# Kernel tuning notes

Measured on AMD Instinct MI355X. Metric: run time of the kernel, lower is better.

The kernel has to match this reference:

```python
import jax, jax.numpy as jnp
import numpy as np

N, K, D = 131072, 4096, 64


def setup_inputs() -> dict:
    key = jax.random.key(0)
    k1, k2 = jax.random.split(key)
    z_e_x = jax.random.normal(k1, (N, D), dtype=jnp.float32)
    codebook = jax.random.normal(k2, (K, D), dtype=jnp.float32)
    return {"z_e_x": z_e_x, "codebook": codebook}


def reference(z_e_x, codebook):
    inputs_sqr = jnp.sum(z_e_x * z_e_x, axis=1, keepdims=True)       # [N, 1]
    codebook_sqr = jnp.sum(codebook * codebook, axis=1)              # [K]
    distances = inputs_sqr + codebook_sqr - 2.0 * jnp.einsum(
        'nd,kd->nk', z_e_x, codebook)                                # [N, K]
    indices = jnp.argmin(distances, axis=1)                          # [N]
    codes = jnp.take(codebook, indices, axis=0)                      # [N, D]
    # Straight-through path: grads pass to z_e_x, not to codebook
    z_q_x_st = z_e_x + jax.lax.stop_gradient(codes - z_e_x)
    # Differentiable-codebook path (index_select on live weight)
    z_q_x_bar = codes
    return jnp.stack([z_q_x_st, z_q_x_bar])                          # [2, N, D]
```

## Files before the change

### kernel.cpp

```cpp
#include <hip/hip_runtime.h>

typedef __attribute__((ext_vector_type(8))) short short8;
typedef __attribute__((ext_vector_type(4))) float f32x4;

constexpr int N_ROWS = 131072;
constexpr int K_CB   = 4096;
constexpr int D_DIM  = 64;
constexpr float EPS_MARGIN = 2.0e-3f;

constexpr size_t CTR_OFF   = 0;
constexpr size_t CSQ_OFF   = 64;
constexpr size_t CBH_OFF   = 16512;
constexpr size_t CBL_OFF   = CBH_OFF + 524288;
constexpr size_t BESTI_OFF = CBL_OFF + 524288;
constexpr size_t LIST_OFF  = BESTI_OFF + 524288;

#define MFMA(a, b, c) __builtin_amdgcn_mfma_f32_16x16x32_bf16((a), (b), (c), 0, 0, 0)

__device__ __forceinline__ unsigned short f2bf(float f) {
    unsigned int u = __builtin_bit_cast(unsigned int, f);
    u = (u + 0x7fffu + ((u >> 16) & 1u)) >> 16;
    return (unsigned short)u;
}
__device__ __forceinline__ float bf2f(unsigned short h) {
    return __builtin_bit_cast(float, ((unsigned int)h) << 16);
}

__device__ __forceinline__ short8 ldfrag(const unsigned char* smbase, int row, int lane, int ks) {
    const int slot = (((lane >> 4) + ks * 4) ^ (lane & 7));
    uint4 v = *(const uint4*)(smbase + row * 128 + slot * 16);
    return __builtin_bit_cast(short8, v);
}

__global__ __launch_bounds__(256)
void prep_csq(const float* __restrict__ cb, float* __restrict__ csq) {
    const int k = blockIdx.x * 256 + threadIdx.x;
    const float4* row = (const float4*)(cb + (size_t)k * D_DIM);
    float s = 0.f;
    #pragma unroll
    for (int i = 0; i < 16; ++i) {
        float4 v = row[i];
        s = fmaf(v.x, v.x, s); s = fmaf(v.y, v.y, s);
        s = fmaf(v.z, v.z, s); s = fmaf(v.w, v.w, s);
    }
    csq[k] = s;
}

__global__ __launch_bounds__(256)
void prep_split(const float* __restrict__ cb, unsigned char* __restrict__ cbh,
                unsigned char* __restrict__ cbl) {
    const int id  = blockIdx.x * 256 + threadIdx.x;
    const int row = id >> 3, s = id & 7;
    const float4* src = (const float4*)(cb + (size_t)row * D_DIM + s * 8);
    float4 v0 = src[0], v1 = src[1];
    float f[8] = {v0.x, v0.y, v0.z, v0.w, v1.x, v1.y, v1.z, v1.w};
    unsigned int hw[4], lw[4];
    #pragma unroll
    for (int i = 0; i < 4; ++i) {
        unsigned short h0 = f2bf(f[2*i]),     l0 = f2bf(f[2*i]     - bf2f(h0));
        unsigned short h1 = f2bf(f[2*i + 1]), l1 = f2bf(f[2*i + 1] - bf2f(h1));
        hw[i] = (unsigned int)h0 | ((unsigned int)h1 << 16);
        lw[i] = (unsigned int)l0 | ((unsigned int)l1 << 16);
    }
    const int slot = s ^ (row & 7);
    *(uint4*)(cbh + (size_t)row * 128 + slot * 16) = make_uint4(hw[0], hw[1], hw[2], hw[3]);
    *(uint4*)(cbl + (size_t)row * 128 + slot * 16) = make_uint4(lw[0], lw[1], lw[2], lw[3]);
}

__global__ void init_counter(int* counter) { if (threadIdx.x == 0) *counter = 0; }

__device__ __forceinline__ void stage_tile(const unsigned char* __restrict__ cbh,
                                           const unsigned char* __restrict__ cbl,
                                           const float* __restrict__ csqg,
                                           unsigned char* sm, int kt, int wid, int lane) {
    const unsigned char* sh = cbh + (size_t)kt * 128;
    const unsigned char* sl = cbl + (size_t)kt * 128;
    #pragma unroll
    for (int p = 0; p < 4; ++p) {
        const int chunk = wid * 4 + p;
        __builtin_amdgcn_global_load_lds(
            (const __attribute__((address_space(1))) void*)(sh + chunk * 1024 + lane * 16),
            (__attribute__((address_space(3))) void*)(sm + chunk * 1024), 16, 0, 0);
    }
    #pragma unroll
    for (int p = 0; p < 4; ++p) {
        const int chunk = wid * 4 + p;
        __builtin_amdgcn_global_load_lds(
            (const __attribute__((address_space(1))) void*)(sl + chunk * 1024 + lane * 16),
            (__attribute__((address_space(3))) void*)(sm + 16384 + chunk * 1024), 16, 0, 0);
    }
    if (wid < 2) {
        __builtin_amdgcn_global_load_lds(
            (const __attribute__((address_space(1))) void*)(csqg + kt + wid * 64 + lane),
            (__attribute__((address_space(3))) void*)(sm + 32768 + wid * 256), 4, 0, 0);
    }
}

__global__ __launch_bounds__(256, 2)
void vq_main_mfma(const float* __restrict__ z,
                  const float* __restrict__ cb,
                  const unsigned char* __restrict__ cbh,
                  const unsigned char* __restrict__ cbl,
                  const float* __restrict__ csqg,
                  int* __restrict__ besti, int* __restrict__ list,
                  int* __restrict__ counter, float* __restrict__ out) {
    __shared__ __align__(16) unsigned char sm[2][33792];
    const int t = threadIdx.x, lane = t & 63, wid = t >> 6;
    const int n0 = blockIdx.x * 128;
    const int wbase = wid * 32;

    #pragma unroll
    for (int p = 0; p < 4; ++p) {
        const int id = t + p * 256;
        const int row = id >> 3, s = id & 7;
        const float4* src = (const float4*)(z + (size_t)(n0 + row) * D_DIM + s * 8);
        float4 v0 = src[0], v1 = src[1];
        float f[8] = {v0.x, v0.y, v0.z, v0.w, v1.x, v1.y, v1.z, v1.w};
        unsigned int hw[4], lw[4];
        #pragma unroll
        for (int i = 0; i < 4; ++i) {
            unsigned short h0 = f2bf(f[2*i]),     l0 = f2bf(f[2*i]     - bf2f(h0));
            unsigned short h1 = f2bf(f[2*i + 1]), l1 = f2bf(f[2*i + 1] - bf2f(h1));
            hw[i] = (unsigned int)h0 | ((unsigned int)h1 << 16);
            lw[i] = (unsigned int)l0 | ((unsigned int)l1 << 16);
        }
        const int slot = s ^ (row & 7);
        *(uint4*)(&sm[0][row * 128 + slot * 16])         = make_uint4(hw[0], hw[1], hw[2], hw[3]);
        *(uint4*)(&sm[0][16384 + row * 128 + slot * 16]) = make_uint4(lw[0], lw[1], lw[2], lw[3]);
    }
    __syncthreads();

    short8 ah[2][2], al[2][2];
    #pragma unroll
    for (int m = 0; m < 2; ++m)
        #pragma unroll
        for (int ks = 0; ks < 2; ++ks) {
            const int row = wbase + m * 16 + (lane & 15);
            ah[m][ks] = ldfrag(&sm[0][0],     row, lane, ks);
            al[m][ks] = ldfrag(&sm[0][16384], row, lane, ks);
        }
    __syncthreads();

    float b1[2][4], b2[2][4]; int i1[2][4];
    #pragma unroll
    for (int m = 0; m < 2; ++m)
        #pragma unroll
        for (int r = 0; r < 4; ++r) { b1[m][r] = __builtin_inff(); b2[m][r] = __builtin_inff(); i1[m][r] = 0; }

    stage_tile(cbh, cbl, csqg, &sm[0][0], 0, wid, lane);
    __syncthreads();
    int cur = 0;
    for (int kt = 0; kt < K_CB; kt += 128) {
        if (kt + 128 < K_CB)
            stage_tile(cbh, cbl, csqg, &sm[cur ^ 1][0], kt + 128, wid, lane);
        const unsigned char* bhp = &sm[cur][0];
        const unsigned char* blp = &sm[cur][16384];
        const float* cs_l = (const float*)&sm[cur][32768];
        #pragma unroll 2
        for (int c = 0; c < 8; ++c) {
            const int brow = c * 16 + (lane & 15);
            short8 bh0 = ldfrag(bhp, brow, lane, 0), bh1 = ldfrag(bhp, brow, lane, 1);
            short8 bl0 = ldfrag(blp, brow, lane, 0), bl1 = ldfrag(blp, brow, lane, 1);
            const float cs = cs_l[c * 16 + (lane & 15)];
            const int idx = kt + c * 16 + (lane & 15);
            #pragma unroll
            for (int m = 0; m < 2; ++m) {
                f32x4 a0 = {0.f, 0.f, 0.f, 0.f}, a1 = {0.f, 0.f, 0.f, 0.f};
                a0 = MFMA(ah[m][0], bh0, a0);
                a1 = MFMA(ah[m][1], bh1, a1);
                a0 = MFMA(al[m][0], bh0, a0);
                a1 = MFMA(al[m][1], bh1, a1);
                a0 = MFMA(ah[m][0], bl0, a0);
                a1 = MFMA(ah[m][1], bl1, a1);
                a0 = MFMA(al[m][0], bl0, a0);
                a1 = MFMA(al[m][1], bl1, a1);
                #pragma unroll
                for (int r = 0; r < 4; ++r) {
                    const float d = fmaf(a0[r] + a1[r], -2.f, cs);
                    const bool lt = d < b1[m][r];
                    b2[m][r] = fminf(b2[m][r], lt ? b1[m][r] : d);
                    b1[m][r] = lt ? d : b1[m][r];
                    i1[m][r] = lt ? idx : i1[m][r];
                }
            }
        }
        __syncthreads();
        cur ^= 1;
    }

    int* bidx_lds = (int*)&sm[0][0];
    #pragma unroll
    for (int m = 0; m < 2; ++m)
        #pragma unroll
        for (int r = 0; r < 4; ++r) {
            float v1 = b1[m][r], v2 = b2[m][r]; int j1 = i1[m][r];
            #pragma unroll
            for (int msk = 1; msk < 16; msk <<= 1) {
                const float ov1 = __shfl_xor(v1, msk);
                const int   oj1 = __shfl_xor(j1, msk);
                const float ov2 = __shfl_xor(v2, msk);
                const bool take = (ov1 < v1) || (ov1 == v1 && oj1 < j1);
                const float nv2 = fminf(take ? v1 : v2, take ? ov2 : ov1);
                v1 = take ? ov1 : v1; j1 = take ? oj1 : j1; v2 = nv2;
            }
            if ((lane & 15) == 0) {
                const int rloc = wbase + m * 16 + (lane >> 4) * 4 + r;
                const int row = n0 + rloc;
                besti[row] = j1;
                bidx_lds[rloc] = j1;
                if (v2 - v1 < EPS_MARGIN) {
                    const int p = atomicAdd(counter, 1);
                    list[p] = row;
                }
            }
        }
    __syncthreads();

    const float4* cb4 = (const float4*)cb;
    float4* out4 = (float4*)out;
    #pragma unroll
    for (int p = 0; p < 8; ++p) {
        const int id  = t + p * 256;
        const int row = id >> 4, c4 = id & 15;
        const int k = bidx_lds[row];
        const float4 v = cb4[(size_t)k * 16 + c4];
        out4[(size_t)(n0 + row) * 16 + c4] = v;
        out4[(size_t)N_ROWS * 16 + (size_t)(n0 + row) * 16 + c4] = v;
    }
}

__global__ __launch_bounds__(256)
void repair_kernel(const float* __restrict__ z, const float* __restrict__ cb,
                   const float* __restrict__ csq, const int* __restrict__ list,
                   const int* __restrict__ counter, int* __restrict__ besti,
                   float* __restrict__ out) {
    __shared__ float xs[64];
    __shared__ float rv[4];
    __shared__ int   ri[4];
    __shared__ int   fi_s;
    const int cnt = counter[0];
    const int t = threadIdx.x;
    for (int e = blockIdx.x; e < cnt; e += gridDim.x) {
        const int row = list[e];
        __syncthreads();
        if (t < 64) xs[t] = z[(size_t)row * D_DIM + t];
        __syncthreads();
        float bv = __builtin_inff(); int bi = 0x7fffffff;
        for (int k = t; k < K_CB; k += 256) {
            const float4* cr = (const float4*)(cb + (size_t)k * D_DIM);
            float dot = 0.f;
            #pragma unroll
            for (int i = 0; i < 16; ++i) {
                float4 v = cr[i];
                dot = fmaf(v.x, xs[i * 4 + 0], dot);
                dot = fmaf(v.y, xs[i * 4 + 1], dot);
                dot = fmaf(v.z, xs[i * 4 + 2], dot);
                dot = fmaf(v.w, xs[i * 4 + 3], dot);
            }
            const float d = fmaf(dot, -2.f, csq[k]);
            if (d < bv) { bv = d; bi = k; }
        }
        #pragma unroll
        for (int msk = 1; msk < 64; msk <<= 1) {
            const float ov = __shfl_xor(bv, msk);
            const int   oi = __shfl_xor(bi, msk);
            if (ov < bv || (ov == bv && oi < bi)) { bv = ov; bi = oi; }
        }
        if ((t & 63) == 0) { rv[t >> 6] = bv; ri[t >> 6] = bi; }
        __syncthreads();
        if (t == 0) {
            float fb = rv[0]; int fi = ri[0];
            #pragma unroll
            for (int w = 1; w < 4; ++w)
                if (rv[w] < fb || (rv[w] == fb && ri[w] < fi)) { fb = rv[w]; fi = ri[w]; }
            besti[row] = fi;
            fi_s = fi;
        }
        __syncthreads();
        if (t < 32) {
            const int dest = t >> 4, c4 = t & 15;
            const float4 v = ((const float4*)cb)[(size_t)fi_s * 16 + c4];
            float4* dst = (float4*)out + (size_t)dest * N_ROWS * 16 + (size_t)row * 16 + c4;
            *dst = v;
        }
        __syncthreads();
    }
}

extern "C" void kernel_launch(void* const* d_in, const int* in_sizes, int n_in,
                              void* d_out, int out_size, void* d_ws, size_t ws_size,
                              hipStream_t stream) {
    const float* z  = (const float*)d_in[0];
    const float* cb = (const float*)d_in[1];
    float* out = (float*)d_out;
    unsigned char* ws = (unsigned char*)d_ws;

    int*   counter = (int*)(ws + CTR_OFF);
    float* csq     = (float*)(ws + CSQ_OFF);
    unsigned char* cbh = ws + CBH_OFF;
    unsigned char* cbl = ws + CBL_OFF;
    int* besti = (int*)(ws + BESTI_OFF);
    int* list  = (int*)(ws + LIST_OFF);

    prep_csq<<<K_CB / 256, 256, 0, stream>>>(cb, csq);
    prep_split<<<(K_CB * 8) / 256, 256, 0, stream>>>(cb, cbh, cbl);
    init_counter<<<1, 64, 0, stream>>>(counter);
    vq_main_mfma<<<N_ROWS / 128, 256, 0, stream>>>(z, cb, cbh, cbl, csq, besti, list, counter, out);
    repair_kernel<<<1024, 256, 0, stream>>>(z, cb, csq, list, counter, besti, out);
}
```

Before: 287.6 us.

## Drop low*low MFMA term, halve codebook tile and raise occupancy

Result: faster. 255.9 us (-11.0%).

```diff
diff --git a/kernel.cpp b/kernel.cpp
--- a/kernel.cpp
+++ b/kernel.cpp
@@ -6,14 +6,13 @@
 constexpr int N_ROWS = 131072;
 constexpr int K_CB   = 4096;
 constexpr int D_DIM  = 64;
-constexpr float EPS_MARGIN = 2.0e-3f;
+constexpr float EPS_MARGIN = 2.5e-3f;
 
 constexpr size_t CTR_OFF   = 0;
 constexpr size_t CSQ_OFF   = 64;
 constexpr size_t CBH_OFF   = 16512;
 constexpr size_t CBL_OFF   = CBH_OFF + 524288;
-constexpr size_t BESTI_OFF = CBL_OFF + 524288;
-constexpr size_t LIST_OFF  = BESTI_OFF + 524288;
+constexpr size_t LIST_OFF  = CBL_OFF + 524288;
 
 #define MFMA(a, b, c) __builtin_amdgcn_mfma_f32_16x16x32_bf16((a), (b), (c), 0, 0, 0)
 
@@ -76,35 +75,36 @@
     const unsigned char* sh = cbh + (size_t)kt * 128;
     const unsigned char* sl = cbl + (size_t)kt * 128;
     #pragma unroll
-    for (int p = 0; p < 4; ++p) {
-        const int chunk = wid * 4 + p;
+    for (int p = 0; p < 2; ++p) {
+        const int chunk = wid * 2 + p;
         __builtin_amdgcn_global_load_lds(
             (const __attribute__((address_space(1))) void*)(sh + chunk * 1024 + lane * 16),
             (__attribute__((address_space(3))) void*)(sm + chunk * 1024), 16, 0, 0);
     }
     #pragma unroll
-    for (int p = 0; p < 4; ++p) {
-        const int chunk = wid * 4 + p;
+    for (int p = 0; p < 2; ++p) {
+        const int chunk = wid * 2 + p;
         __builtin_amdgcn_global_load_lds(
             (const __attribute__((address_space(1))) void*)(sl + chunk * 1024 + lane * 16),
-            (__attribute__((address_space(3))) void*)(sm + 16384 + chunk * 1024), 16, 0, 0);
-    }
-    if (wid < 2) {
+            (__attribute__((address_space(3))) void*)(sm + 8192 + chunk * 1024), 16, 0, 0);
+    }
+    if (wid == 0) {
         __builtin_amdgcn_global_load_lds(
-            (const __attribute__((address_space(1))) void*)(csqg + kt + wid * 64 + lane),
-            (__attribute__((address_space(3))) void*)(sm + 32768 + wid * 256), 4, 0, 0);
-    }
-}
-
-__global__ __launch_bounds__(256, 2)
+            (const __attribute__((address_space(1))) void*)(csqg + kt + lane),
+            (__attribute__((address_space(3))) void*)(sm + 16384), 4, 0, 0);
+    }
+}
+
+__global__ __launch_bounds__(256, 4)
 void vq_main_mfma(const float* __restrict__ z,
                   const float* __restrict__ cb,
                   const unsigned char* __restrict__ cbh,
                   const unsigned char* __restrict__ cbl,
                   const float* __restrict__ csqg,
-                  int* __restrict__ besti, int* __restrict__ list,
+                  int* __restrict__ list,
                   int* __restrict__ counter, float* __restrict__ out) {
-    __shared__ __align__(16) unsigned char sm[2][33792];
+    __shared__ __align__(16) unsigned char sm[2][16640];
+    unsigned char* smf = &sm[0][0];
     const int t = threadIdx.x, lane = t & 63, wid = t >> 6;
     const int n0 = blockIdx.x * 128;
     const int wbase = wid * 32;
@@ -125,8 +125,8 @@
             lw[i] = (unsigned int)l0 | ((unsigned int)l1 << 16);
         }
         const int slot = s ^ (row & 7);
-        *(uint4*)(&sm[0][row * 128 + slot * 16])         = make_uint4(hw[0], hw[1], hw[2], hw[3]);
-        *(uint4*)(&sm[0][16384 + row * 128 + slot * 16]) = make_uint4(lw[0], lw[1], lw[2], lw[3]);
+        *(uint4*)(smf + row * 128 + slot * 16)         = make_uint4(hw[0], hw[1], hw[2], hw[3]);
+        *(uint4*)(smf + 16384 + row * 128 + slot * 16) = make_uint4(lw[0], lw[1], lw[2], lw[3]);
     }
     __syncthreads();
 
@@ -136,8 +136,8 @@
         #pragma unroll
         for (int ks = 0; ks < 2; ++ks) {
             const int row = wbase + m * 16 + (lane & 15);
-            ah[m][ks] = ldfrag(&sm[0][0],     row, lane, ks);
-            al[m][ks] = ldfrag(&sm[0][16384], row, lane, ks);
+            ah[m][ks] = ldfrag(smf,         row, lane, ks);
+            al[m][ks] = ldfrag(smf + 16384, row, lane, ks);
         }
     __syncthreads();
 
@@ -150,14 +150,14 @@
     stage_tile(cbh, cbl, csqg, &sm[0][0], 0, wid, lane);
     __syncthreads();
     int cur = 0;
-    for (int kt = 0; kt < K_CB; kt += 128) {
-        if (kt + 128 < K_CB)
-            stage_tile(cbh, cbl, csqg, &sm[cur ^ 1][0], kt + 128, wid, lane);
+    for (int kt = 0; kt < K_CB; kt += 64) {
+        if (kt + 64 < K_CB)
+            stage_tile(cbh, cbl, csqg, &sm[cur ^ 1][0], kt + 64, wid, lane);
         const unsigned char* bhp = &sm[cur][0];
-        const unsigned char* blp = &sm[cur][16384];
-        const float* cs_l = (const float*)&sm[cur][32768];
+        const unsigned char* blp = &sm[cur][8192];
+        const float* cs_l = (const float*)&sm[cur][16384];
         #pragma unroll 2
-        for (int c = 0; c < 8; ++c) {
+        for (int c = 0; c < 4; ++c) {
             const int brow = c * 16 + (lane & 15);
             short8 bh0 = ldfrag(bhp, brow, lane, 0), bh1 = ldfrag(bhp, brow, lane, 1);
             short8 bl0 = ldfrag(blp, brow, lane, 0), bl1 = ldfrag(blp, brow, lane, 1);
@@ -172,8 +172,6 @@
                 a1 = MFMA(al[m][1], bh1, a1);
                 a0 = MFMA(ah[m][0], bl0, a0);
                 a1 = MFMA(ah[m][1], bl1, a1);
-                a0 = MFMA(al[m][0], bl0, a0);
-                a1 = MFMA(al[m][1], bl1, a1);
                 #pragma unroll
                 for (int r = 0; r < 4; ++r) {
                     const float d = fmaf(a0[r] + a1[r], -2.f, cs);
@@ -205,12 +203,10 @@
             }
             if ((lane & 15) == 0) {
                 const int rloc = wbase + m * 16 + (lane >> 4) * 4 + r;
-                const int row = n0 + rloc;
-                besti[row] = j1;
                 bidx_lds[rloc] = j1;
                 if (v2 - v1 < EPS_MARGIN) {
                     const int p = atomicAdd(counter, 1);
-                    list[p] = row;
+                    list[p] = n0 + rloc;
                 }
             }
         }
@@ -232,8 +228,7 @@
 __global__ __launch_bounds__(256)
 void repair_kernel(const float* __restrict__ z, const float* __restrict__ cb,
                    const float* __restrict__ csq, const int* __restrict__ list,
-                   const int* __restrict__ counter, int* __restrict__ besti,
-                   float* __restrict__ out) {
+                   const int* __restrict__ counter, float* __restrict__ out) {
     __shared__ float xs[64];
     __shared__ float rv[4];
     __shared__ int   ri[4];
@@ -273,7 +268,6 @@
             #pragma unroll
             for (int w = 1; w < 4; ++w)
                 if (rv[w] < fb || (rv[w] == fb && ri[w] < fi)) { fb = rv[w]; fi = ri[w]; }
-            besti[row] = fi;
             fi_s = fi;
         }
         __syncthreads();
@@ -299,12 +293,11 @@
     float* csq     = (float*)(ws + CSQ_OFF);
     unsigned char* cbh = ws + CBH_OFF;
     unsigned char* cbl = ws + CBL_OFF;
-    int* besti = (int*)(ws + BESTI_OFF);
     int* list  = (int*)(ws + LIST_OFF);
 
     prep_csq<<<K_CB / 256, 256, 0, stream>>>(cb, csq);
     prep_split<<<(K_CB * 8) / 256, 256, 0, stream>>>(cb, cbh, cbl);
     init_counter<<<1, 64, 0, stream>>>(counter);
-    vq_main_mfma<<<N_ROWS / 128, 256, 0, stream>>>(z, cb, cbh, cbl, csq, besti, list, counter, out);
-    repair_kernel<<<1024, 256, 0, stream>>>(z, cb, csq, list, counter, besti, out);
-}
+    vq_main_mfma<<<N_ROWS / 128, 256, 0, stream>>>(z, cb, cbh, cbl, csq, list, counter, out);
+    repair_kernel<<<1024, 256, 0, stream>>>(z, cb, csq, list, counter, out);
+}
```
